# Kernel optimization log

Hardware: AMD Instinct MI355X
Metric: run time of the kernel (lower is better)

The kernel has to match this reference:

```python
import jax, jax.numpy as jnp
import numpy as np

N_NODES = 100000


def _gcn_layer(x, W, b, src, dst, n):
    # symmetric normalization (add_self_loops=False): deg = in-degree at dst
    deg = jax.ops.segment_sum(jnp.ones_like(src, dtype=x.dtype), dst, num_segments=n)
    dis = jnp.where(deg > 0, jax.lax.rsqrt(jnp.maximum(deg, 1.0)), 0.0)
    h = x @ W                                    # [N, out]
    norm = dis[src] * dis[dst]                   # [E]
    msg = h[src] * norm[:, None]                 # [E, out]
    out = jax.ops.segment_sum(msg, dst, num_segments=n)
    return out + b


def setup_inputs() -> dict:
    key = jax.random.key(0)
    k1, k2, k3, k4, k5, k6 = jax.random.split(key, 6)
    F_IN, HID, OUT = 64, 64, 2
    x = jax.random.normal(k1, (N_NODES, F_IN), dtype=jnp.float32)
    edge_index = jax.random.randint(k2, (2, 1600000), 0, N_NODES, dtype=jnp.int64)
    s1 = 1.0 / np.sqrt(2 * F_IN)
    s2 = 1.0 / np.sqrt(HID)
    W1 = jax.random.uniform(k3, (2 * F_IN, HID), jnp.float32, -s1, s1)
    b1 = jax.random.uniform(k4, (HID,), jnp.float32, -s1, s1)
    W2 = jax.random.uniform(k5, (HID, OUT), jnp.float32, -s2, s2)
    b2 = jax.random.uniform(k6, (OUT,), jnp.float32, -s2, s2)
    return {"x": x, "edge_index": edge_index, "W1": W1, "b1": b1, "W2": W2, "b2": b2}


def reference(x, edge_index, W1, b1, W2, b2):
    n = x.shape[0]
    src, dst = edge_index[0], edge_index[1]
    # global mean pool broadcast to every node, concat on feature dim -> [N, 2F]
    mean = jnp.mean(x, axis=0, keepdims=True)
    complete = jnp.concatenate([x, jnp.broadcast_to(mean, x.shape)], axis=1)
    h = _gcn_layer(complete, W1, b1, src, dst, n)
    h = jax.nn.relu(h)
    out = _gcn_layer(h, W2, b2, src, dst, n)
    return out
```

## Files before the change

kernel.cpp:

```cpp
#include <hip/hip_runtime.h>


#define NPB        256
#define NPB_SHIFT  8
#define BKTS       512
#define BKT_CAP    5120
#define CHUNK      4096
#define EPT        8
#define CS_BLK     128
#define CUR_STRIDE 32

using bf16x8 = __attribute__((ext_vector_type(8))) short;
using f32x4  = __attribute__((ext_vector_type(4))) float;

__device__ __forceinline__ unsigned short f2bf(float v) {
    unsigned u = __float_as_uint(v);
    u += 0x7FFFu + ((u >> 16) & 1u);
    return (unsigned short)(u >> 16);
}
__device__ __forceinline__ float bfu_lo(unsigned u) { return __uint_as_float(u << 16); }
__device__ __forceinline__ float bfu_hi(unsigned u) { return __uint_as_float(u & 0xFFFF0000u); }

__global__ __launch_bounds__(512) void bucketAC_kernel(
        const int* __restrict__ src, const int* __restrict__ dst,
        int e, unsigned* __restrict__ pairs, int* __restrict__ cursor,
        const float* __restrict__ x, float* __restrict__ sums,
        const float* __restrict__ W1, unsigned short* __restrict__ wtg,
        unsigned short* __restrict__ xbf, int n) {
    int tid = threadIdx.x;
    if (blockIdx.x < CS_BLK) {
        __shared__ float4 s4[512];
        int cb = blockIdx.x;
        const float4* x4 = (const float4*)x;
        int total4 = n * 16;
        float4 acc = make_float4(0.f, 0.f, 0.f, 0.f);
        for (int i = cb * 512 + tid; i < total4; i += CS_BLK * 512) {
            float4 v = x4[i];
            acc.x += v.x; acc.y += v.y; acc.z += v.z; acc.w += v.w;
            ushort4 hv;
            hv.x = f2bf(v.x); hv.y = f2bf(v.y); hv.z = f2bf(v.z); hv.w = f2bf(v.w);
            *(ushort4*)&xbf[(size_t)i * 4] = hv;
        }
        s4[tid] = acc;
        __syncthreads();
        if (tid < 16) {
            float4 v = s4[tid];
            for (int k = 1; k < 32; ++k) {
                float4 w = s4[tid + 16 * k];
                v.x += w.x; v.y += w.y; v.z += w.z; v.w += w.w;
            }
            atomicAdd(&sums[tid * 4 + 0], v.x);
            atomicAdd(&sums[tid * 4 + 1], v.y);
            atomicAdd(&sums[tid * 4 + 2], v.z);
            atomicAdd(&sums[tid * 4 + 3], v.w);
        }
        return;
    }
    if (blockIdx.x == CS_BLK) {
        for (int i = tid; i < 4096; i += 512) {
            int k = i >> 6, j = i & 63;
            wtg[j * 64 + k] = f2bf(W1[k * 64 + j]);
        }
        return;
    }
    __shared__ int cnt[BKTS], gpos[BKTS];
    __shared__ int wsumA[8];
    __shared__ unsigned stage[CHUNK];
    __shared__ unsigned short bb[CHUNK];
    int chunkStart = (blockIdx.x - CS_BLK - 1) * CHUNK;
    int v = e - chunkStart;
    if (v > CHUNK) v = CHUNK;
    cnt[tid] = 0;
    __syncthreads();
    int myb[EPT], myoff[EPT];
    unsigned myp[EPT];
#pragma unroll
    for (int t = 0; t < EPT; ++t) {
        int i = chunkStart + t * 512 + tid;
        myb[t] = -1;
        if (i < e) {
            int s = src[i], d = dst[i];
            myb[t] = d >> NPB_SHIFT;
            myp[t] = ((unsigned)s << NPB_SHIFT) | (unsigned)(d & (NPB - 1));
            myoff[t] = atomicAdd(&cnt[myb[t]], 1);
        }
    }
    __syncthreads();
    int lane = tid & 63, wvi = tid >> 6;
    int myCnt = cnt[tid];
    int sv = myCnt;
#pragma unroll
    for (int off = 1; off < 64; off <<= 1) {
        int t = __shfl_up(sv, off, 64);
        if (lane >= off) sv += t;
    }
    if (lane == 63) wsumA[wvi] = sv;
    __syncthreads();
    int wbase = 0;
#pragma unroll
    for (int k = 0; k < 8; ++k) if (k < wvi) wbase += wsumA[k];
    int excl = sv + wbase - myCnt;
    if (myCnt > 0) {
        int gb = atomicAdd(&cursor[tid * CUR_STRIDE], myCnt);
        gpos[tid] = tid * BKT_CAP + gb - excl;
    }
    cnt[tid] = excl;
    __syncthreads();
#pragma unroll
    for (int t = 0; t < EPT; ++t) {
        if (myb[t] >= 0) {
            int p = cnt[myb[t]] + myoff[t];
            stage[p] = myp[t];
            bb[p] = (unsigned short)myb[t];
        }
    }
    __syncthreads();
    for (int j = tid; j < v; j += 512) {
        int bk = bb[j];
        int wi = gpos[bk] + j;
        if (wi < (bk + 1) * BKT_CAP) pairs[wi] = stage[j];
    }
}

__global__ __launch_bounds__(512) void csrBG_kernel(
        const unsigned* __restrict__ pairs, const int* __restrict__ cursor,
        float* __restrict__ dis, int* __restrict__ rowstart,
        int* __restrict__ eidx, int n,
        const float* __restrict__ sums, const float* __restrict__ W1,
        const unsigned short* __restrict__ wtg, const unsigned short* __restrict__ xbf,
        unsigned short* __restrict__ h1s) {
    __shared__ int ldeg[NPB];
    __shared__ int lcur[NPB];
    __shared__ int wred[8], wsum[8];
    __shared__ __align__(16) float cv[64];
    __shared__ unsigned short Ws[64 * 72];
    __shared__ unsigned short Xs[2][64 * 72];
    float* disl = (float*)ldeg;
    int b = blockIdx.x;
    int tid = threadIdx.x;
    int lane = tid & 63;
    int wvi = tid >> 6;
    int node0 = b << NPB_SHIFT;
    int nl = n - node0;
    if (nl > NPB) nl = NPB;
    int cnt_b = cursor[b * CUR_STRIDE];
    if (cnt_b > BKT_CAP) cnt_b = BKT_CAP;
    if (tid < NPB) ldeg[tid] = 0;
    int c = (tid < b) ? cursor[tid * CUR_STRIDE] : 0;
#pragma unroll
    for (int off = 1; off < 64; off <<= 1) c += __shfl_xor(c, off, 64);
    if (lane == 0) wred[wvi] = c;
    __syncthreads();
    const unsigned* mp = pairs + (size_t)b * BKT_CAP;
    for (int i = tid; i < cnt_b; i += 512)
        atomicAdd(&ldeg[mp[i] & (NPB - 1)], 1);
    int ebase = 0;
#pragma unroll
    for (int k = 0; k < 8; ++k) ebase += wred[k];
    __syncthreads();
    int mydeg = (tid < NPB) ? ldeg[tid] : 0;
    int sv = mydeg;
#pragma unroll
    for (int off = 1; off < 64; off <<= 1) {
        int t = __shfl_up(sv, off, 64);
        if (lane >= off) sv += t;
    }
    if (lane == 63) wsum[wvi] = sv;
    __syncthreads();
    int wbase = 0;
#pragma unroll
    for (int k = 0; k < 8; ++k) if (k < wvi) wbase += wsum[k];
    int excl = sv + wbase - mydeg;
    if (tid < NPB) {
        lcur[tid] = excl;
        if (tid < nl) rowstart[node0 + tid] = ebase + excl;
        float dv = mydeg > 0 ? rsqrtf((float)mydeg) : 0.f;
        disl[tid] = dv;
        if (tid < nl) dis[node0 + tid] = dv;
    }
    if (tid == 0 && node0 + NPB >= n)
        rowstart[n] = ebase + cnt_b;
    __syncthreads();
    for (int i = tid; i < cnt_b; i += 512) {
        unsigned p = mp[i];
        int pos = atomicAdd(&lcur[p & (NPB - 1)], 1);
        eidx[ebase + pos] = (int)(p >> NPB_SHIFT);
    }
    if (tid < 64) {
        float inv_n = 1.0f / (float)n;
        float acc = 0.f;
        for (int k = 0; k < 64; ++k) acc += (sums[k] * inv_n) * W1[(64 + k) * 64 + tid];
        cv[tid] = acc;
    }
    for (int i = tid; i < 1024; i += 512) {
        int j = i >> 4, k4 = (i & 15) * 4;
        *(ushort4*)&Ws[j * 72 + k4] = *(const ushort4*)&wtg[j * 64 + k4];
    }
    int wv = wvi;
    int tile = wv >> 2;
    int w4 = wv & 3;
    int l15 = lane & 15;
    int quad = lane >> 4;
#pragma unroll
    for (int it = 0; it < 2; ++it) {
        __syncthreads();
        for (int i = tid; i < 1024; i += 512) {
            int r = i >> 3, c8 = (i & 7) * 8;
            int gr = node0 + it * 128 + r;
            bf16x8 hv = {0, 0, 0, 0, 0, 0, 0, 0};
            if (gr < n) hv = *(const bf16x8*)&xbf[(size_t)gr * 64 + c8];
            *(bf16x8*)&Xs[r >> 6][(r & 63) * 72 + c8] = hv;
        }
        __syncthreads();
        int xrow = w4 * 16 + l15;
        f32x4 acc0 = {0.f, 0.f, 0.f, 0.f}, acc1 = acc0, acc2 = acc0, acc3 = acc0;
#pragma unroll
        for (int ks = 0; ks < 2; ++ks) {
            bf16x8 bfrag = *(const bf16x8*)&Xs[tile][xrow * 72 + ks * 32 + quad * 8];
            bf16x8 a0 = *(const bf16x8*)&Ws[(0 * 16 + l15) * 72 + ks * 32 + quad * 8];
            bf16x8 a1 = *(const bf16x8*)&Ws[(1 * 16 + l15) * 72 + ks * 32 + quad * 8];
            bf16x8 a2 = *(const bf16x8*)&Ws[(2 * 16 + l15) * 72 + ks * 32 + quad * 8];
            bf16x8 a3 = *(const bf16x8*)&Ws[(3 * 16 + l15) * 72 + ks * 32 + quad * 8];
            acc0 = __builtin_amdgcn_mfma_f32_16x16x32_bf16(a0, bfrag, acc0, 0, 0, 0);
            acc1 = __builtin_amdgcn_mfma_f32_16x16x32_bf16(a1, bfrag, acc1, 0, 0, 0);
            acc2 = __builtin_amdgcn_mfma_f32_16x16x32_bf16(a2, bfrag, acc2, 0, 0, 0);
            acc3 = __builtin_amdgcn_mfma_f32_16x16x32_bf16(a3, bfrag, acc3, 0, 0, 0);
        }
        int lrow = it * 128 + tile * 64 + xrow;
        int grow = node0 + lrow;
        if (grow < n) {
            float dv = disl[lrow];
            const float4* c4 = (const float4*)cv;
            f32x4 accs[4] = {acc0, acc1, acc2, acc3};
#pragma unroll
            for (int t = 0; t < 4; ++t) {
                float4 cj = c4[t * 4 + quad];
                ushort4 hs;
                hs.x = f2bf((accs[t][0] + cj.x) * dv);
                hs.y = f2bf((accs[t][1] + cj.y) * dv);
                hs.z = f2bf((accs[t][2] + cj.z) * dv);
                hs.w = f2bf((accs[t][3] + cj.w) * dv);
                *(ushort4*)&h1s[(size_t)grow * 64 + t * 16 + quad * 4] = hs;
            }
        }
    }
}

__global__ void gather1_kernel(const int* __restrict__ rowstart,
                               const int* __restrict__ eidx, const float* __restrict__ dis,
                               const unsigned short* __restrict__ h1s,
                               const float* __restrict__ b1, const float* __restrict__ W2,
                               float* __restrict__ h2s, int n) {
    int lane = threadIdx.x & 63;
    int node = blockIdx.x * 4 + (threadIdx.x >> 6);
    if (node >= n) return;
    int rs = rowstart[node];
    int re = rowstart[node + 1];
    int dn = re - rs;
    int m = dn < 64 ? dn : 64;
    int eHeld = (lane < m) ? eidx[rs + lane] : 0;
    int sub = lane >> 5;
    int fp  = (lane & 31) * 2;
    float ax = 0.f, ay = 0.f;
    int j = 0;
    for (; j + 16 <= m; j += 16) {
        int s0 = __shfl(eHeld, j + 0 + sub, 64);
        int s1 = __shfl(eHeld, j + 2 + sub, 64);
        int s2 = __shfl(eHeld, j + 4 + sub, 64);
        int s3 = __shfl(eHeld, j + 6 + sub, 64);
        int s4 = __shfl(eHeld, j + 8 + sub, 64);
        int s5 = __shfl(eHeld, j + 10 + sub, 64);
        int s6 = __shfl(eHeld, j + 12 + sub, 64);
        int s7 = __shfl(eHeld, j + 14 + sub, 64);
        unsigned u0 = *(const unsigned*)&h1s[((size_t)s0 << 6) + fp];
        unsigned u1 = *(const unsigned*)&h1s[((size_t)s1 << 6) + fp];
        unsigned u2 = *(const unsigned*)&h1s[((size_t)s2 << 6) + fp];
        unsigned u3 = *(const unsigned*)&h1s[((size_t)s3 << 6) + fp];
        unsigned u4 = *(const unsigned*)&h1s[((size_t)s4 << 6) + fp];
        unsigned u5 = *(const unsigned*)&h1s[((size_t)s5 << 6) + fp];
        unsigned u6 = *(const unsigned*)&h1s[((size_t)s6 << 6) + fp];
        unsigned u7 = *(const unsigned*)&h1s[((size_t)s7 << 6) + fp];
        ax += (bfu_lo(u0) + bfu_lo(u1)) + (bfu_lo(u2) + bfu_lo(u3))
            + (bfu_lo(u4) + bfu_lo(u5)) + (bfu_lo(u6) + bfu_lo(u7));
        ay += (bfu_hi(u0) + bfu_hi(u1)) + (bfu_hi(u2) + bfu_hi(u3))
            + (bfu_hi(u4) + bfu_hi(u5)) + (bfu_hi(u6) + bfu_hi(u7));
    }
    for (; j + 8 <= m; j += 8) {
        int s0 = __shfl(eHeld, j + 0 + sub, 64);
        int s1 = __shfl(eHeld, j + 2 + sub, 64);
        int s2 = __shfl(eHeld, j + 4 + sub, 64);
        int s3 = __shfl(eHeld, j + 6 + sub, 64);
        unsigned u0 = *(const unsigned*)&h1s[((size_t)s0 << 6) + fp];
        unsigned u1 = *(const unsigned*)&h1s[((size_t)s1 << 6) + fp];
        unsigned u2 = *(const unsigned*)&h1s[((size_t)s2 << 6) + fp];
        unsigned u3 = *(const unsigned*)&h1s[((size_t)s3 << 6) + fp];
        ax += (bfu_lo(u0) + bfu_lo(u1)) + (bfu_lo(u2) + bfu_lo(u3));
        ay += (bfu_hi(u0) + bfu_hi(u1)) + (bfu_hi(u2) + bfu_hi(u3));
    }
    for (; j + 4 <= m; j += 4) {
        int s0 = __shfl(eHeld, j + 0 + sub, 64);
        int s1 = __shfl(eHeld, j + 2 + sub, 64);
        unsigned u0 = *(const unsigned*)&h1s[((size_t)s0 << 6) + fp];
        unsigned u1 = *(const unsigned*)&h1s[((size_t)s1 << 6) + fp];
        ax += bfu_lo(u0) + bfu_lo(u1);
        ay += bfu_hi(u0) + bfu_hi(u1);
    }
    for (; j < m; j += 2) {
        int jj = j + sub;
        int s = __shfl(eHeld, jj < m ? jj : 0, 64);
        if (jj < m) {
            unsigned u = *(const unsigned*)&h1s[((size_t)s << 6) + fp];
            ax += bfu_lo(u);
            ay += bfu_hi(u);
        }
    }
    for (int t = 64; t < dn; ++t) {
        if (sub == 0) {
            int s = eidx[rs + t];
            unsigned u = *(const unsigned*)&h1s[((size_t)s << 6) + fp];
            ax += bfu_lo(u);
            ay += bfu_hi(u);
        }
    }
    ax += __shfl_xor(ax, 32, 64);
    ay += __shfl_xor(ay, 32, 64);
    float di = dis[node];
    float2 bv = ((const float2*)b1)[lane & 31];
    float4 w = ((const float4*)W2)[lane & 31];
    float t0 = fmaxf(di * ax + bv.x, 0.f);
    float t1 = fmaxf(di * ay + bv.y, 0.f);
    float v0 = t0 * w.x + t1 * w.z;
    float v1 = t0 * w.y + t1 * w.w;
#pragma unroll
    for (int off = 1; off <= 16; off <<= 1) {
        v0 += __shfl_xor(v0, off, 64);
        v1 += __shfl_xor(v1, off, 64);
    }
    if (lane == 0) {
        h2s[(size_t)node * 2 + 0] = di * v0;
        h2s[(size_t)node * 2 + 1] = di * v1;
    }
}

__global__ void gather2_kernel(const int* __restrict__ rowstart,
                               const int* __restrict__ eidx, const float* __restrict__ dis,
                               const float2* __restrict__ h2s, const float* __restrict__ b2,
                               float2* __restrict__ out, int n) {
    int tid = threadIdx.x;
    int node = blockIdx.x * 16 + (tid >> 4);
    if (node >= n) return;
    int el = tid & 15;
    int rs = rowstart[node];
    int dn = rowstart[node + 1] - rs;
    float ax = 0.f, ay = 0.f;
    for (int t = el; t < dn; t += 16) {
        int s = eidx[rs + t];
        float2 h = h2s[s];
        ax += h.x;
        ay += h.y;
    }
#pragma unroll
    for (int off = 1; off <= 8; off <<= 1) {
        ax += __shfl_xor(ax, off, 64);
        ay += __shfl_xor(ay, off, 64);
    }
    if (el == 0) {
        float di = dis[node];
        out[node] = make_float2(di * ax + b2[0], di * ay + b2[1]);
    }
}

extern "C" void kernel_launch(void* const* d_in, const int* in_sizes, int n_in,
                              void* d_out, int out_size, void* d_ws, size_t ws_size,
                              hipStream_t stream) {
    const float* x  = (const float*)d_in[0];
    const int*   ei = (const int*)d_in[1];
    const float* W1 = (const float*)d_in[2];
    const float* b1 = (const float*)d_in[3];
    const float* W2 = (const float*)d_in[4];
    const float* b2 = (const float*)d_in[5];
    float2* out = (float2*)d_out;

    const int n = in_sizes[0] / 64;
    const int e = in_sizes[1] / 2;
    const int* srcI = ei;
    const int* dstI = ei + e;
    const int nbkt = (n + NPB - 1) >> NPB_SHIFT;

    char* p = (char*)d_ws;
    int* rowstart = (int*)p;    p += ((size_t)(n + 1) * 4 + 255) & ~255ull;
    float* dis    = (float*)p;  p += ((size_t)n * 4 + 255) & ~255ull;
    float* sums   = (float*)p;
    int* cursor   = (int*)(p + 256);
    size_t zsize  = 256 + (size_t)nbkt * CUR_STRIDE * 4;
    char* zbase   = p;          p += (zsize + 255) & ~255ull;
    unsigned short* wtg = (unsigned short*)p;  p += (4096 * 2 + 255) & ~255ull;
    unsigned short* xbf = (unsigned short*)p;  p += ((size_t)n * 64 * 2 + 255) & ~255ull;
    int* eidx     = (int*)p;    p += ((size_t)e * 4 + 255) & ~255ull;
    unsigned* pairs = (unsigned*)p;  p += ((size_t)nbkt * BKT_CAP * 4 + 255) & ~255ull;
    unsigned short* h1s = (unsigned short*)p;  p += ((size_t)n * 64 * 2 + 255) & ~255ull;
    float* h2s    = (float*)p;

    hipMemsetAsync(zbase, 0, zsize, stream);

    const int nchunks = (e + CHUNK - 1) / CHUNK;

    bucketAC_kernel<<<CS_BLK + 1 + nchunks, 512, 0, stream>>>(srcI, dstI, e, pairs, cursor,
                                                              x, sums, W1, wtg, xbf, n);
    csrBG_kernel<<<nbkt, 512, 0, stream>>>(pairs, cursor, dis, rowstart, eidx, n,
                                           sums, W1, wtg, xbf, h1s);
    gather1_kernel<<<(n + 3) / 4, 256, 0, stream>>>(rowstart, eidx, dis, h1s, b1, W2, h2s, n);
    gather2_kernel<<<(n + 15) / 16, 256, 0, stream>>>(rowstart, eidx, dis, (const float2*)h2s,
                                                      b2, out, n);
}
```

Measured before the change: 182.5 us.

## Replace bucketed two-pass CSR build with global histogram, scan and atomic fill

Replaces the bucket-by-destination-block staging (pairs buffer with per-bucket capacity) with a classic CSR construction: a global atomic degree histogram, two-kernel prefix scan, and a fill kernel that scatters source indices using global atomics on per-node cursors. The GEMM producing h1s is split into its own kernel that reads dis from global memory. This removes the fixed bucket capacity limit and the shared-memory staging, but trades them for 1.6M global atomics on random addresses twice and more kernel launches, and edge order within rows becomes nondeterministic.

```diff
diff --git a/kernel.cpp b/kernel.cpp
--- a/kernel.cpp
+++ b/kernel.cpp
@@ -3,12 +3,10 @@
 
 #define NPB        256
 #define NPB_SHIFT  8
-#define BKTS       512
-#define BKT_CAP    5120
 #define CHUNK      4096
 #define EPT        8
 #define CS_BLK     128
-#define CUR_STRIDE 32
+#define FILL_BLK   1024
 
 using bf16x8 = __attribute__((ext_vector_type(8))) short;
 using f32x4  = __attribute__((ext_vector_type(4))) float;
@@ -21,9 +19,8 @@
 __device__ __forceinline__ float bfu_lo(unsigned u) { return __uint_as_float(u << 16); }
 __device__ __forceinline__ float bfu_hi(unsigned u) { return __uint_as_float(u & 0xFFFF0000u); }
 
-__global__ __launch_bounds__(512) void bucketAC_kernel(
-        const int* __restrict__ src, const int* __restrict__ dst,
-        int e, unsigned* __restrict__ pairs, int* __restrict__ cursor,
+__global__ __launch_bounds__(512) void histAC_kernel(
+        const int* __restrict__ dst, int e, int* __restrict__ deg,
         const float* __restrict__ x, float* __restrict__ sums,
         const float* __restrict__ W1, unsigned short* __restrict__ wtg,
         unsigned short* __restrict__ xbf, int n) {
@@ -63,129 +60,85 @@
         }
         return;
     }
-    __shared__ int cnt[BKTS], gpos[BKTS];
-    __shared__ int wsumA[8];
-    __shared__ unsigned stage[CHUNK];
-    __shared__ unsigned short bb[CHUNK];
     int chunkStart = (blockIdx.x - CS_BLK - 1) * CHUNK;
-    int v = e - chunkStart;
-    if (v > CHUNK) v = CHUNK;
-    cnt[tid] = 0;
-    __syncthreads();
-    int myb[EPT], myoff[EPT];
-    unsigned myp[EPT];
 #pragma unroll
     for (int t = 0; t < EPT; ++t) {
         int i = chunkStart + t * 512 + tid;
-        myb[t] = -1;
-        if (i < e) {
-            int s = src[i], d = dst[i];
-            myb[t] = d >> NPB_SHIFT;
-            myp[t] = ((unsigned)s << NPB_SHIFT) | (unsigned)(d & (NPB - 1));
-            myoff[t] = atomicAdd(&cnt[myb[t]], 1);
-        }
-    }
+        if (i < e) atomicAdd(&deg[dst[i]], 1);
+    }
+}
+
+__global__ __launch_bounds__(256) void scan1_kernel(
+        const int* __restrict__ deg, int* __restrict__ bsum, int n) {
+    __shared__ int ws[4];
+    int b = blockIdx.x, tid = threadIdx.x;
+    int gid = (b << NPB_SHIFT) + tid;
+    int v = (gid < n) ? deg[gid] : 0;
+#pragma unroll
+    for (int off = 1; off < 64; off <<= 1) v += __shfl_xor(v, off, 64);
+    if ((tid & 63) == 0) ws[tid >> 6] = v;
     __syncthreads();
+    if (tid == 0) bsum[b] = ws[0] + ws[1] + ws[2] + ws[3];
+}
+
+__global__ __launch_bounds__(256) void scan2_kernel(
+        const int* __restrict__ deg, const int* __restrict__ bsum,
+        int* __restrict__ rowstart, int* __restrict__ cur,
+        float* __restrict__ dis, int n) {
+    __shared__ int ws[4], sb[4];
+    int b = blockIdx.x, tid = threadIdx.x;
     int lane = tid & 63, wvi = tid >> 6;
-    int myCnt = cnt[tid];
-    int sv = myCnt;
+    int gid = (b << NPB_SHIFT) + tid;
+    int c = 0;
+    for (int k = tid; k < b; k += 256) c += bsum[k];
+#pragma unroll
+    for (int off = 1; off < 64; off <<= 1) c += __shfl_xor(c, off, 64);
+    if (lane == 0) sb[wvi] = c;
+    int v = (gid < n) ? deg[gid] : 0;
+    int sv = v;
 #pragma unroll
     for (int off = 1; off < 64; off <<= 1) {
         int t = __shfl_up(sv, off, 64);
         if (lane >= off) sv += t;
     }
-    if (lane == 63) wsumA[wvi] = sv;
+    if (lane == 63) ws[wvi] = sv;
     __syncthreads();
+    int ebase = sb[0] + sb[1] + sb[2] + sb[3];
     int wbase = 0;
 #pragma unroll
-    for (int k = 0; k < 8; ++k) if (k < wvi) wbase += wsumA[k];
-    int excl = sv + wbase - myCnt;
-    if (myCnt > 0) {
-        int gb = atomicAdd(&cursor[tid * CUR_STRIDE], myCnt);
-        gpos[tid] = tid * BKT_CAP + gb - excl;
-    }
-    cnt[tid] = excl;
-    __syncthreads();
-#pragma unroll
-    for (int t = 0; t < EPT; ++t) {
-        if (myb[t] >= 0) {
-            int p = cnt[myb[t]] + myoff[t];
-            stage[p] = myp[t];
-            bb[p] = (unsigned short)myb[t];
-        }
-    }
-    __syncthreads();
-    for (int j = tid; j < v; j += 512) {
-        int bk = bb[j];
-        int wi = gpos[bk] + j;
-        if (wi < (bk + 1) * BKT_CAP) pairs[wi] = stage[j];
-    }
-}
-
-__global__ __launch_bounds__(512) void csrBG_kernel(
-        const unsigned* __restrict__ pairs, const int* __restrict__ cursor,
-        float* __restrict__ dis, int* __restrict__ rowstart,
-        int* __restrict__ eidx, int n,
+    for (int k = 0; k < 4; ++k) if (k < wvi) wbase += ws[k];
+    int excl = ebase + wbase + sv - v;
+    if (gid < n) {
+        rowstart[gid] = excl;
+        cur[gid] = excl;
+        dis[gid] = (v > 0) ? rsqrtf((float)v) : 0.f;
+    } else if (gid == n) {
+        rowstart[n] = excl;
+    }
+}
+
+__global__ __launch_bounds__(256) void fill_kernel(
+        const int* __restrict__ src, const int* __restrict__ dst,
+        int* __restrict__ cur, int* __restrict__ eidx, int e) {
+    int stride = gridDim.x * 256;
+    for (int i = blockIdx.x * 256 + threadIdx.x; i < e; i += stride) {
+        int s = src[i], d = dst[i];
+        int pos = atomicAdd(&cur[d], 1);
+        eidx[pos] = s;
+    }
+}
+
+__global__ __launch_bounds__(512) void gemmH_kernel(
         const float* __restrict__ sums, const float* __restrict__ W1,
         const unsigned short* __restrict__ wtg, const unsigned short* __restrict__ xbf,
-        unsigned short* __restrict__ h1s) {
-    __shared__ int ldeg[NPB];
-    __shared__ int lcur[NPB];
-    __shared__ int wred[8], wsum[8];
+        const float* __restrict__ dis, unsigned short* __restrict__ h1s, int n) {
     __shared__ __align__(16) float cv[64];
     __shared__ unsigned short Ws[64 * 72];
     __shared__ unsigned short Xs[2][64 * 72];
-    float* disl = (float*)ldeg;
     int b = blockIdx.x;
     int tid = threadIdx.x;
     int lane = tid & 63;
-    int wvi = tid >> 6;
     int node0 = b << NPB_SHIFT;
-    int nl = n - node0;
-    if (nl > NPB) nl = NPB;
-    int cnt_b = cursor[b * CUR_STRIDE];
-    if (cnt_b > BKT_CAP) cnt_b = BKT_CAP;
-    if (tid < NPB) ldeg[tid] = 0;
-    int c = (tid < b) ? cursor[tid * CUR_STRIDE] : 0;
-#pragma unroll
-    for (int off = 1; off < 64; off <<= 1) c += __shfl_xor(c, off, 64);
-    if (lane == 0) wred[wvi] = c;
-    __syncthreads();
-    const unsigned* mp = pairs + (size_t)b * BKT_CAP;
-    for (int i = tid; i < cnt_b; i += 512)
-        atomicAdd(&ldeg[mp[i] & (NPB - 1)], 1);
-    int ebase = 0;
-#pragma unroll
-    for (int k = 0; k < 8; ++k) ebase += wred[k];
-    __syncthreads();
-    int mydeg = (tid < NPB) ? ldeg[tid] : 0;
-    int sv = mydeg;
-#pragma unroll
-    for (int off = 1; off < 64; off <<= 1) {
-        int t = __shfl_up(sv, off, 64);
-        if (lane >= off) sv += t;
-    }
-    if (lane == 63) wsum[wvi] = sv;
-    __syncthreads();
-    int wbase = 0;
-#pragma unroll
-    for (int k = 0; k < 8; ++k) if (k < wvi) wbase += wsum[k];
-    int excl = sv + wbase - mydeg;
-    if (tid < NPB) {
-        lcur[tid] = excl;
-        if (tid < nl) rowstart[node0 + tid] = ebase + excl;
-        float dv = mydeg > 0 ? rsqrtf((float)mydeg) : 0.f;
-        disl[tid] = dv;
-        if (tid < nl) dis[node0 + tid] = dv;
-    }
-    if (tid == 0 && node0 + NPB >= n)
-        rowstart[n] = ebase + cnt_b;
-    __syncthreads();
-    for (int i = tid; i < cnt_b; i += 512) {
-        unsigned p = mp[i];
-        int pos = atomicAdd(&lcur[p & (NPB - 1)], 1);
-        eidx[ebase + pos] = (int)(p >> NPB_SHIFT);
-    }
     if (tid < 64) {
         float inv_n = 1.0f / (float)n;
         float acc = 0.f;
@@ -196,7 +149,7 @@
         int j = i >> 4, k4 = (i & 15) * 4;
         *(ushort4*)&Ws[j * 72 + k4] = *(const ushort4*)&wtg[j * 64 + k4];
     }
-    int wv = wvi;
+    int wv = tid >> 6;
     int tile = wv >> 2;
     int w4 = wv & 3;
     int l15 = lane & 15;
@@ -229,7 +182,7 @@
         int lrow = it * 128 + tile * 64 + xrow;
         int grow = node0 + lrow;
         if (grow < n) {
-            float dv = disl[lrow];
+            float dv = dis[grow];
             const float4* c4 = (const float4*)cv;
             f32x4 accs[4] = {acc0, acc1, acc2, acc3};
 #pragma unroll
@@ -390,14 +343,15 @@
     char* p = (char*)d_ws;
     int* rowstart = (int*)p;    p += ((size_t)(n + 1) * 4 + 255) & ~255ull;
     float* dis    = (float*)p;  p += ((size_t)n * 4 + 255) & ~255ull;
-    float* sums   = (float*)p;
-    int* cursor   = (int*)(p + 256);
-    size_t zsize  = 256 + (size_t)nbkt * CUR_STRIDE * 4;
+    int* deg      = (int*)p;
+    float* sums   = (float*)(p + (size_t)n * 4);
+    size_t zsize  = (size_t)n * 4 + 256;
     char* zbase   = p;          p += (zsize + 255) & ~255ull;
+    int* cur      = (int*)p;    p += ((size_t)n * 4 + 255) & ~255ull;
+    int* bsum     = (int*)p;    p += ((size_t)nbkt * 4 + 255) & ~255ull;
     unsigned short* wtg = (unsigned short*)p;  p += (4096 * 2 + 255) & ~255ull;
     unsigned short* xbf = (unsigned short*)p;  p += ((size_t)n * 64 * 2 + 255) & ~255ull;
     int* eidx     = (int*)p;    p += ((size_t)e * 4 + 255) & ~255ull;
-    unsigned* pairs = (unsigned*)p;  p += ((size_t)nbkt * BKT_CAP * 4 + 255) & ~255ull;
     unsigned short* h1s = (unsigned short*)p;  p += ((size_t)n * 64 * 2 + 255) & ~255ull;
     float* h2s    = (float*)p;
 
@@ -405,10 +359,12 @@
 
     const int nchunks = (e + CHUNK - 1) / CHUNK;
 
-    bucketAC_kernel<<<CS_BLK + 1 + nchunks, 512, 0, stream>>>(srcI, dstI, e, pairs, cursor,
-                                                              x, sums, W1, wtg, xbf, n);
-    csrBG_kernel<<<nbkt, 512, 0, stream>>>(pairs, cursor, dis, rowstart, eidx, n,
-                                           sums, W1, wtg, xbf, h1s);
+    histAC_kernel<<<CS_BLK + 1 + nchunks, 512, 0, stream>>>(dstI, e, deg, x, sums,
+                                                            W1, wtg, xbf, n);
+    scan1_kernel<<<nbkt, 256, 0, stream>>>(deg, bsum, n);
+    scan2_kernel<<<nbkt, 256, 0, stream>>>(deg, bsum, rowstart, cur, dis, n);
+    fill_kernel<<<FILL_BLK, 256, 0, stream>>>(srcI, dstI, cur, eidx, e);
+    gemmH_kernel<<<nbkt, 512, 0, stream>>>(sums, W1, wtg, xbf, dis, h1s, n);
     gather1_kernel<<<(n + 3) / 4, 256, 0, stream>>>(rowstart, eidx, dis, h1s, b1, W2, h2s, n);
     gather2_kernel<<<(n + 15) / 16, 256, 0, stream>>>(rowstart, eidx, dis, (const float2*)h2s,
                                                       b2, out, n);
```

Result: slower. 345.9 us (+89.6%).
